# Kernel tuning notes

Hardware: AMD Instinct MI355X
Metric: run time of the kernel (lower is better)

Reference implementation:

```python
import jax, jax.numpy as jnp
import numpy as np

N = 50000      # nodes
E = 800000     # edges (avg degree 16)
C_IN = 64
C_OUT = 64
H = 32         # hidden_nf (hard-coded in module)
L = 4          # egnn_clean.EGNN default n_layers


def _lin(key, fan_in, fan_out):
    s = 1.0 / np.sqrt(fan_in)
    kw, kb = jax.random.split(key)
    w = jax.random.uniform(kw, (fan_in, fan_out), jnp.float32, -s, s)
    b = jax.random.uniform(kb, (fan_out,), jnp.float32, -s, s)
    return w, b


def _stack(key, fan_in, fan_out):
    ws, bs = zip(*[_lin(jax.random.fold_in(key, l), fan_in, fan_out) for l in range(L)])
    return jnp.stack(ws), jnp.stack(bs)


def setup_inputs() -> dict:
    key = jax.random.key(0)
    k = jax.random.split(key, 16)
    inp = {
        'data': jax.random.normal(k[0], (N, C_IN), jnp.float32),
        'pos': jax.random.normal(k[1], (N, 2), jnp.float32),
        'edge_attr': jax.random.normal(k[2], (E, 1), jnp.float32),
        't': jnp.ones((1,), jnp.float32),
        'row': jax.random.randint(k[3], (E,), 0, N),
        'col': jax.random.randint(k[4], (E,), 0, N),
    }
    inp['emb_in_w'], inp['emb_in_b'] = _lin(k[5], C_IN + 1, H)
    inp['emb_out_w'], inp['emb_out_b'] = _lin(k[6], H, C_OUT)
    inp['edge_w1'], inp['edge_b1'] = _stack(k[7], 2 * H + 2, H)  # [h_i, h_j, radial, edge_attr]
    inp['edge_w2'], inp['edge_b2'] = _stack(k[8], H, H)
    inp['node_w1'], inp['node_b1'] = _stack(k[9], 2 * H, H)
    inp['node_w2'], inp['node_b2'] = _stack(k[10], H, H)
    inp['coord_w1'], inp['coord_b1'] = _stack(k[11], H, H)
    lim = 0.001 * np.sqrt(6.0 / (H + 1))  # xavier_uniform gain=0.001, no bias
    inp['coord_w2'] = jax.random.uniform(k[12], (L, H, 1), jnp.float32, -lim, lim)
    return inp


def _egnn(data, pos, edge_attr, t, emb_in_w, emb_in_b, edge_w1, edge_b1, edge_w2, edge_b2,
          node_w1, node_b1, node_w2, node_b2, coord_w1, coord_b1, coord_w2,
          emb_out_w, emb_out_b, row, col):
    n = data.shape[0]
    silu = jax.nn.silu
    # prepend time channel; pad 2D coords with a zero z-column
    h = jnp.concatenate([jnp.broadcast_to(t.reshape(1, 1), (n, 1)), data], axis=1)  # [N, C_IN+1]
    x = jnp.concatenate([pos, jnp.zeros((n, 1), pos.dtype)], axis=1)                # [N, 3]
    h = h @ emb_in_w + emb_in_b                                                     # [N, H]
    ones_e = jnp.ones((row.shape[0], 1), x.dtype)
    cnt = jnp.maximum(jax.ops.segment_sum(ones_e, row, num_segments=n), 1.0)        # [N,1] clamp(min=1)
    for l in range(L):
        diff = x[row] - x[col]                                    # [E, 3]
        radial = jnp.sum(diff * diff, axis=1, keepdims=True)      # [E, 1]
        ein = jnp.concatenate([h[row], h[col], radial, edge_attr], axis=1)  # [E, 2H+2]
        m = silu(silu(ein @ edge_w1[l] + edge_b1[l]) @ edge_w2[l] + edge_b2[l])  # edge MLP [E, H]
        # equivariant coordinate update (coords_agg='mean')
        phi = silu(m @ coord_w1[l] + coord_b1[l]) @ coord_w2[l]   # [E, 1]
        x = x + jax.ops.segment_sum(diff * phi, row, num_segments=n) / cnt
        # node update (sum aggregation, residual)
        agg = jax.ops.segment_sum(m, row, num_segments=n)         # [N, H]
        upd = silu(jnp.concatenate([h, agg], axis=1) @ node_w1[l] + node_b1[l]) @ node_w2[l] + node_b2[l]
        h = h + upd
    return h @ emb_out_w + emb_out_b                              # [N, C_OUT]


def reference(data, pos, edge_attr, t, emb_in_w, emb_in_b, edge_w1, edge_b1, edge_w2, edge_b2,
              node_w1, node_b1, node_w2, node_b2, coord_w1, coord_b1, coord_w2,
              emb_out_w, emb_out_b, row, col):
    return _egnn(data, pos, edge_attr, t, emb_in_w, emb_in_b, edge_w1, edge_b1, edge_w2, edge_b2,
                 node_w1, node_b1, node_w2, node_b2, coord_w1, coord_b1, coord_w2,
                 emb_out_w, emb_out_b, row, col)
```

## Files before the change

### kernel.cpp

```cpp
#include <hip/hip_runtime.h>
#include <hip/hip_fp16.h>

#define NN 50000
#define NE 800000
#define CIN 64
#define COUT 64
#define HD 32
#define NL 4
#define NBUK 196
#define BUKSH 8
#define EPB 3125
#define MAXB 4864
#define BLKE 128

typedef float f32x4 __attribute__((ext_vector_type(4)));
typedef _Float16 half8 __attribute__((ext_vector_type(8)));

__device__ __forceinline__ float silu_f(float v) {
    return v * __builtin_amdgcn_rcpf(1.0f + __expf(-v));
}

__global__ __launch_bounds__(256) void embed_kernel(
    const float* __restrict__ data, const float* __restrict__ pos,
    const float* __restrict__ tptr,
    const float* __restrict__ W, const float* __restrict__ b,
    const float* __restrict__ eW1_0,
    float* __restrict__ h, float* __restrict__ x4,
    __half* __restrict__ Hrh, __half* __restrict__ Hch,
    int* __restrict__ bcnt, float* __restrict__ aggM, float* __restrict__ aggX4)
{
    int n = blockIdx.x * 256 + threadIdx.x;
    if (n >= NN) return;
    float t = tptr[0];
    float d[CIN];
    const float4* dp = (const float4*)(data + (size_t)n * CIN);
#pragma unroll
    for (int i = 0; i < CIN / 4; i++) {
        float4 v = dp[i];
        d[4*i+0] = v.x; d[4*i+1] = v.y; d[4*i+2] = v.z; d[4*i+3] = v.w;
    }
    float acc[HD];
#pragma unroll
    for (int j = 0; j < HD; j++) acc[j] = fmaf(t, W[j], b[j]);
#pragma unroll
    for (int i = 0; i < CIN; i++) {
        float a = d[i];
#pragma unroll
        for (int j = 0; j < HD; j++) acc[j] = fmaf(a, W[(i + 1) * HD + j], acc[j]);
    }
    float4* hp = (float4*)(h + (size_t)n * HD);
#pragma unroll
    for (int j = 0; j < HD / 4; j++)
        hp[j] = make_float4(acc[4*j], acc[4*j+1], acc[4*j+2], acc[4*j+3]);
    ((float4*)x4)[n] = make_float4(pos[n*2+0], pos[n*2+1], 0.0f, 0.0f);

    float a1[HD], a2[HD];
#pragma unroll
    for (int j = 0; j < HD; j++) { a1[j] = 0.0f; a2[j] = 0.0f; }
#pragma unroll
    for (int i = 0; i < HD; i++) {
        float z = acc[i];
#pragma unroll
        for (int j = 0; j < HD; j++) {
            a1[j] = fmaf(z, eW1_0[i * HD + j], a1[j]);
            a2[j] = fmaf(z, eW1_0[(HD + i) * HD + j], a2[j]);
        }
    }
    int w1[16], w2[16];
#pragma unroll
    for (int q = 0; q < 16; q++) {
        __half2 p1 = __floats2half2_rn(a1[2*q], a1[2*q+1]);
        __half2 p2 = __floats2half2_rn(a2[2*q], a2[2*q+1]);
        w1[q] = *(int*)&p1;
        w2[q] = *(int*)&p2;
    }
    int4* rp = (int4*)(Hrh + (size_t)n * HD);
    int4* cp = (int4*)(Hch + (size_t)n * HD);
#pragma unroll
    for (int q = 0; q < 4; q++) {
        rp[q] = make_int4(w1[4*q], w1[4*q+1], w1[4*q+2], w1[4*q+3]);
        cp[q] = make_int4(w2[4*q], w2[4*q+1], w2[4*q+2], w2[4*q+3]);
    }

    if (n < NBUK) bcnt[n] = 0;
    float4 z4 = make_float4(0.f, 0.f, 0.f, 0.f);
    float4* za = (float4*)(aggM + (size_t)n * HD);
#pragma unroll
    for (int j = 0; j < HD/4; j++) za[j] = z4;
    ((float4*)aggX4)[n] = z4;
}

__global__ __launch_bounds__(128) void prep_kernel(
    const float* __restrict__ eW2, const float* __restrict__ cW1,
    __half* __restrict__ w2B, __half* __restrict__ cW1B)
{
    int l  = blockIdx.x;
    int nt = threadIdx.x >> 6;
    int wl = threadIdx.x & 63;
    int rsel = wl & 15, ksel = wl >> 4;
#pragma unroll
    for (int e = 0; e < 8; e++) {
        int k = 8 * ksel + e;
        int j = 16 * nt + rsel;
        size_t o = ((size_t)(l * 2 + nt) * 64 + wl) * 8 + e;
        w2B[o]  = __float2half(eW2[(size_t)l * HD * HD + k * HD + j]);
        cW1B[o] = __float2half(cW1[(size_t)l * HD * HD + k * HD + j]);
    }
}

__global__ __launch_bounds__(256) void sortS1_kernel(
    const int* __restrict__ row, int* __restrict__ bcnt, int* __restrict__ resv)
{
    __shared__ int lb[256];
    int tid = threadIdx.x;
    lb[tid] = 0;
    __syncthreads();
    int base = blockIdx.x * EPB;
    for (int i = tid; i < EPB; i += 256)
        atomicAdd(&lb[row[base + i] >> BUKSH], 1);
    __syncthreads();
    if (tid < NBUK)
        resv[blockIdx.x * NBUK + tid] = atomicAdd(&bcnt[tid], lb[tid]);
}

__global__ __launch_bounds__(256) void sortS2_kernel(
    const int* __restrict__ bcnt, int* __restrict__ bbase)
{
    __shared__ int sd[256];
    int tid = threadIdx.x;
    int v = (tid < NBUK) ? bcnt[tid] : 0;
    sd[tid] = v;
    __syncthreads();
    for (int off = 1; off < 256; off <<= 1) {
        int t = (tid >= off) ? sd[tid - off] : 0;
        __syncthreads();
        sd[tid] += t;
        __syncthreads();
    }
    if (tid < NBUK) bbase[tid] = sd[tid] - v;
    if (tid == 255) bbase[NBUK] = sd[255];
}

__global__ __launch_bounds__(256) void sortS3_kernel(
    const int* __restrict__ row, const int* __restrict__ col,
    const float* __restrict__ eattr,
    const int* __restrict__ bbase, const int* __restrict__ resv,
    int4* __restrict__ tmp)
{
    __shared__ int4 st[EPB];
    __shared__ int lb[256];
    __shared__ int lbex[NBUK];
    __shared__ int lcur[NBUK];
    __shared__ int sd[256];
    int tid = threadIdx.x;
    int base = blockIdx.x * EPB;
    lb[tid] = 0;
    if (tid < NBUK) lcur[tid] = 0;
    __syncthreads();
    for (int i = tid; i < EPB; i += 256)
        atomicAdd(&lb[row[base + i] >> BUKSH], 1);
    __syncthreads();
    int v = lb[tid];
    sd[tid] = v;
    __syncthreads();
    for (int off = 1; off < 256; off <<= 1) {
        int t = (tid >= off) ? sd[tid - off] : 0;
        __syncthreads();
        sd[tid] += t;
        __syncthreads();
    }
    if (tid < NBUK) lbex[tid] = sd[tid] - v;
    __syncthreads();
    for (int i = tid; i < EPB; i += 256) {
        int e = base + i;
        int r = row[e];
        int b = r >> BUKSH;
        int p = lbex[b] + atomicAdd(&lcur[b], 1);
        st[p] = make_int4(r, col[e], __float_as_int(eattr[e]), 0);
    }
    __syncthreads();
    int wid = tid >> 6, lane = tid & 63;
    for (int k = wid; k < NBUK; k += 4) {
        int L = lb[k];
        int g = bbase[k] + resv[blockIdx.x * NBUK + k];
        int o = lbex[k];
        for (int i = lane; i < L; i += 64)
            tmp[g + i] = st[o + i];
    }
}

__global__ __launch_bounds__(256) void sortS4_kernel(
    const int4* __restrict__ tmp, const int* __restrict__ bbase,
    int4* __restrict__ sedge, int* __restrict__ rowstart)
{
    __shared__ int4 st[MAXB];
    __shared__ int lcnt[256], lex[256], lcur[256], sd[256];
    int tid = threadIdx.x;
    int k = blockIdx.x;
    int lo = bbase[k], hi = bbase[k + 1];
    int nE = hi - lo;
    int nodeBase = k << BUKSH;
    lcnt[tid] = 0; lcur[tid] = 0;
    __syncthreads();
    for (int i = tid; i < nE; i += 256)
        atomicAdd(&lcnt[tmp[lo + i].x - nodeBase], 1);
    __syncthreads();
    int v = lcnt[tid];
    sd[tid] = v;
    __syncthreads();
    for (int off = 1; off < 256; off <<= 1) {
        int t = (tid >= off) ? sd[tid - off] : 0;
        __syncthreads();
        sd[tid] += t;
        __syncthreads();
    }
    lex[tid] = sd[tid] - v;
    int n = nodeBase + tid;
    if (n < NN) rowstart[n] = lo + lex[tid];
    if (k == NBUK - 1 && tid == 0) rowstart[NN] = NE;
    __syncthreads();
    for (int i = tid; i < nE; i += 256) {
        int4 e = tmp[lo + i];
        int ln = e.x - nodeBase;
        int p = lex[ln] + atomicAdd(&lcur[ln], 1);
        st[p] = e;
    }
    __syncthreads();
    for (int i = tid; i < nE; i += 256)
        sedge[lo + i] = st[i];
}

__global__ __launch_bounds__(128, 8) void edge_fused_kernel(
    const float* __restrict__ x4,
    const int4* __restrict__ sedge,
    const __half* __restrict__ Hrh, const __half* __restrict__ Hch,
    const float* __restrict__ eW1, const float* __restrict__ eb1,
    const float* __restrict__ eb2,
    const __half* __restrict__ w2Bl, const __half* __restrict__ cW1Bl,
    const float* __restrict__ cb1, const float* __restrict__ cW2,
    const int* __restrict__ rowstart,
    float* __restrict__ aggM, float* __restrict__ aggX4)
{
    __shared__ __align__(16) __half At[BLKE][40];
    __shared__ __half sx[BLKE][4];
    __shared__ float  phib[BLKE];
    __shared__ int snf, snl;
    int tid = threadIdx.x;
    int s_base = blockIdx.x * BLKE;
    int s = s_base + tid;
    int4 ei = sedge[s];
    int r = ei.x, c = ei.y;
    float ea = __int_as_float(ei.z);
    if (tid == 0)        snf = r;
    if (tid == BLKE - 1) snl = r;

    float4 xr = ((const float4*)x4)[r];
    float4 xc = ((const float4*)x4)[c];
    float d0 = xr.x - xc.x, d1 = xr.y - xc.y, d2 = xr.z - xc.z;
    float radial = d0*d0 + d1*d1 + d2*d2;

    const half8* hr8 = (const half8*)(Hrh + (size_t)r * HD);
    const half8* hc8 = (const half8*)(Hch + (size_t)c * HD);
    int wbuf[16];
#pragma unroll
    for (int i = 0; i < 4; i++) {
        half8 s8 = hr8[i] + hc8[i];
#pragma unroll
        for (int kk = 0; kk < 8; kk += 2) {
            int j = 8*i + kk;
            float v0 = (float)s8[kk]   + eb1[j]   + radial * eW1[64*HD+j]   + ea * eW1[65*HD+j];
            float v1 = (float)s8[kk+1] + eb1[j+1] + radial * eW1[64*HD+j+1] + ea * eW1[65*HD+j+1];
            __half2 p = __floats2half2_rn(silu_f(v0), silu_f(v1));
            wbuf[(j >> 1)] = *(int*)&p;
        }
    }
    int4* arow = (int4*)&At[tid][0];
#pragma unroll
    for (int q = 0; q < 4; q++)
        arow[q] = make_int4(wbuf[4*q], wbuf[4*q+1], wbuf[4*q+2], wbuf[4*q+3]);

    int wl = tid & 63;
    int wbase = tid & 64;
    int rsel = wl & 15, ksel = wl >> 4;

    half8 bw0 = ((const half8*)w2Bl)[wl];
    half8 bw1 = ((const half8*)w2Bl)[64 + wl];
    float bc0 = eb2[rsel], bc1 = eb2[16 + rsel];
    f32x4 acc[4][2];
#pragma unroll
    for (int mt = 0; mt < 4; mt++) {
        acc[mt][0] = (f32x4){bc0, bc0, bc0, bc0};
        acc[mt][1] = (f32x4){bc1, bc1, bc1, bc1};
    }
#pragma unroll
    for (int mt = 0; mt < 4; mt++) {
        half8 af = *(const half8*)&At[wbase + 16*mt + rsel][8*ksel];
        acc[mt][0] = __builtin_amdgcn_mfma_f32_16x16x32_f16(af, bw0, acc[mt][0], 0, 0, 0);
        acc[mt][1] = __builtin_amdgcn_mfma_f32_16x16x32_f16(af, bw1, acc[mt][1], 0, 0, 0);
    }
#pragma unroll
    for (int mt = 0; mt < 4; mt++)
#pragma unroll
        for (int nt = 0; nt < 2; nt++)
#pragma unroll
            for (int q = 0; q < 4; q++) {
                float mv = silu_f(acc[mt][nt][q]);
                At[wbase + 16*mt + 4*ksel + q][16*nt + rsel] = __float2half(mv);
            }

    half8 cw0 = ((const half8*)cW1Bl)[wl];
    half8 cw1 = ((const half8*)cW1Bl)[64 + wl];
    float cc0 = cb1[rsel], cc1 = cb1[16 + rsel];
    f32x4 cacc[4][2];
#pragma unroll
    for (int mt = 0; mt < 4; mt++) {
        cacc[mt][0] = (f32x4){cc0, cc0, cc0, cc0};
        cacc[mt][1] = (f32x4){cc1, cc1, cc1, cc1};
    }
#pragma unroll
    for (int mt = 0; mt < 4; mt++) {
        half8 am = *(const half8*)&At[wbase + 16*mt + rsel][8*ksel];
        cacc[mt][0] = __builtin_amdgcn_mfma_f32_16x16x32_f16(am, cw0, cacc[mt][0], 0, 0, 0);
        cacc[mt][1] = __builtin_amdgcn_mfma_f32_16x16x32_f16(am, cw1, cacc[mt][1], 0, 0, 0);
    }

    float cw2a = cW2[rsel], cw2b = cW2[16 + rsel];
    float p[4][4];
#pragma unroll
    for (int mt = 0; mt < 4; mt++)
#pragma unroll
        for (int q = 0; q < 4; q++)
            p[mt][q] = silu_f(cacc[mt][0][q]) * cw2a + silu_f(cacc[mt][1][q]) * cw2b;
#pragma unroll
    for (int dd = 1; dd < 16; dd <<= 1)
#pragma unroll
        for (int mt = 0; mt < 4; mt++)
#pragma unroll
            for (int q = 0; q < 4; q++)
                p[mt][q] += __shfl_xor(p[mt][q], dd);
    if (rsel == 0) {
#pragma unroll
        for (int mt = 0; mt < 4; mt++)
#pragma unroll
            for (int q = 0; q < 4; q++)
                phib[wbase + 16*mt + 4*ksel + q] = p[mt][q];
    }
    float phi = phib[tid];

    *(__half2*)&sx[tid][0] = __floats2half2_rn(d0 * phi, d1 * phi);
    sx[tid][2] = __float2half(d2 * phi);
    __syncthreads();

    int g = tid >> 5, ch = tid & 31;
    int nf = snf, nl = snl;
    for (int node = nf + g; node <= nl; node += 4) {
        int lo = rowstart[node], hi = rowstart[node + 1];
        int clo = lo - s_base; if (clo < 0) clo = 0;
        int chi = hi - s_base; if (chi > BLKE) chi = BLKE;
        if (chi <= clo) continue;
        float am = 0.0f;
        for (int j = clo; j < chi; j++) am += __half2float(At[j][ch]);
        bool interior = (lo >= s_base) && (hi <= s_base + BLKE);
        if (interior) aggM[(size_t)node * HD + ch] = am;
        else          atomicAdd(&aggM[(size_t)node * HD + ch], am);
        if (ch < 3) {
            float ax = 0.0f;
            for (int j = clo; j < chi; j++) ax += __half2float(sx[j][ch]);
            if (interior) aggX4[(size_t)node * 4 + ch] = ax;
            else          atomicAdd(&aggX4[(size_t)node * 4 + ch], ax);
        }
    }
}

__global__ __launch_bounds__(256) void node_fused_kernel(
    float* __restrict__ h, float* __restrict__ x4,
    float* __restrict__ aggM, float* __restrict__ aggX4,
    const int* __restrict__ rowstart,
    const float* __restrict__ nW1, const float* __restrict__ nb1,
    const float* __restrict__ nW2, const float* __restrict__ nb2,
    const float* __restrict__ eW1n,
    __half* __restrict__ Hrh, __half* __restrict__ Hch,
    const float* __restrict__ Wout, const float* __restrict__ bout,
    float* __restrict__ out)
{
    __shared__ float sIn[8][2*HD];
    __shared__ float sU[8][HD];
    __shared__ float sH[8][HD];
    int local = threadIdx.x >> 5;
    int ch    = threadIdx.x & 31;
    int n = blockIdx.x * 8 + local;
    float hv = h[(size_t)n * HD + ch];
    float am = aggM[(size_t)n * HD + ch];
    aggM[(size_t)n * HD + ch] = 0.0f;
    sIn[local][ch]      = hv;
    sIn[local][HD + ch] = am;
    if (ch < 3) {
        int cnt = rowstart[n + 1] - rowstart[n];
        float cf = (cnt < 1) ? 1.0f : (float)cnt;
        x4[(size_t)n * 4 + ch] += aggX4[(size_t)n * 4 + ch] / cf;
        aggX4[(size_t)n * 4 + ch] = 0.0f;
    }
    __syncthreads();
    float u1 = nb1[ch];
#pragma unroll 8
    for (int i = 0; i < 2*HD; i++) u1 = fmaf(sIn[local][i], nW1[i * HD + ch], u1);
    u1 = silu_f(u1);
    sU[local][ch] = u1;
    __syncthreads();
    float u2 = nb2[ch];
#pragma unroll 8
    for (int i = 0; i < HD; i++) u2 = fmaf(sU[local][i], nW2[i * HD + ch], u2);
    float hn = hv + u2;

    if (eW1n != nullptr) {
        h[(size_t)n * HD + ch] = hn;
        sH[local][ch] = hn;
        __syncthreads();
        float a = 0.0f, b = 0.0f;
#pragma unroll 8
        for (int i = 0; i < HD; i++) {
            float z = sH[local][i];
            a = fmaf(z, eW1n[i * HD + ch], a);
            b = fmaf(z, eW1n[(HD + i) * HD + ch], b);
        }
        Hrh[(size_t)n * HD + ch] = __float2half(a);
        Hch[(size_t)n * HD + ch] = __float2half(b);
    } else {
        sH[local][ch] = hn;
        __syncthreads();
        float o0 = bout[ch], o1 = bout[HD + ch];
#pragma unroll 8
        for (int i = 0; i < HD; i++) {
            float z = sH[local][i];
            o0 = fmaf(z, Wout[i * COUT + ch], o0);
            o1 = fmaf(z, Wout[i * COUT + HD + ch], o1);
        }
        out[(size_t)n * COUT + ch]      = o0;
        out[(size_t)n * COUT + HD + ch] = o1;
    }
}

extern "C" void kernel_launch(void* const* d_in, const int* in_sizes, int n_in,
                              void* d_out, int out_size, void* d_ws, size_t ws_size,
                              hipStream_t stream) {
    const float* data      = (const float*)d_in[0];
    const float* pos       = (const float*)d_in[1];
    const float* edge_attr = (const float*)d_in[2];
    const float* tptr      = (const float*)d_in[3];
    const int*   row       = (const int*)d_in[4];
    const int*   col       = (const int*)d_in[5];
    const float* emb_in_w  = (const float*)d_in[6];
    const float* emb_in_b  = (const float*)d_in[7];
    const float* emb_out_w = (const float*)d_in[8];
    const float* emb_out_b = (const float*)d_in[9];
    const float* edge_w1   = (const float*)d_in[10];
    const float* edge_b1   = (const float*)d_in[11];
    const float* edge_w2   = (const float*)d_in[12];
    const float* edge_b2   = (const float*)d_in[13];
    const float* node_w1   = (const float*)d_in[14];
    const float* node_b1   = (const float*)d_in[15];
    const float* node_w2   = (const float*)d_in[16];
    const float* node_b2   = (const float*)d_in[17];
    const float* coord_w1  = (const float*)d_in[18];
    const float* coord_b1  = (const float*)d_in[19];
    const float* coord_w2  = (const float*)d_in[20];
    float* out = (float*)d_out;

    float* ws = (float*)d_ws;
    float* h      = ws;
    float* x4     = ws + 1600000;
    __half* Hrh   = (__half*)(ws + 1800000);
    __half* Hch   = (__half*)(ws + 2600000);
    float* aggM   = ws + 3400000;
    float* aggX4  = ws + 5000000;
    int* rowstart = (int*)(ws + 5200000);
    int* bcnt     = (int*)(ws + 5250004);
    int* bbase    = (int*)(ws + 5250204);
    int* resv     = (int*)(ws + 5250404);
    int4* sedge   = (int4*)(ws + 5400000);
    int4* tmp     = (int4*)(ws + 8600000);
    __half* w2B   = (__half*)(ws + 11800000);
    __half* cW1B  = w2B + (size_t)NL * 1024;

    embed_kernel<<<(NN + 255) / 256, 256, 0, stream>>>(
        data, pos, tptr, emb_in_w, emb_in_b, edge_w1 ,
        h, x4, Hrh, Hch, bcnt, aggM, aggX4);
    prep_kernel<<<NL, 128, 0, stream>>>(edge_w2, coord_w1, w2B, cW1B);
    sortS1_kernel<<<256, 256, 0, stream>>>(row, bcnt, resv);
    sortS2_kernel<<<1, 256, 0, stream>>>(bcnt, bbase);
    sortS3_kernel<<<256, 256, 0, stream>>>(row, col, edge_attr, bbase, resv, tmp);
    sortS4_kernel<<<NBUK, 256, 0, stream>>>(tmp, bbase, sedge, rowstart);

    for (int l = 0; l < NL; l++) {
        edge_fused_kernel<<<NE / BLKE, BLKE, 0, stream>>>(
            x4, sedge, Hrh, Hch,
            edge_w1 + l * (2*HD+2) * HD, edge_b1 + l * HD,
            edge_b2 + l * HD,
            w2B + (size_t)l * 1024, cW1B + (size_t)l * 1024,
            coord_b1 + l * HD, coord_w2 + l * HD,
            rowstart, aggM, aggX4);
        bool lastl = (l + 1 == NL);
        node_fused_kernel<<<NN / 8, 256, 0, stream>>>(
            h, x4, aggM, aggX4, rowstart,
            node_w1 + l * 2 * HD * HD, node_b1 + l * HD,
            node_w2 + l * HD * HD,     node_b2 + l * HD,
            lastl ? nullptr : (edge_w1 + (l + 1) * (2*HD+2) * HD), Hrh, Hch,
            emb_out_w, emb_out_b, lastl ? out : nullptr);
    }
}
```

Measured before the change: 413.3 us.

## Merge prologue kernels and compute bucket offsets inside scatter kernel

Combines embedding, per-block bucket histogram and weight repacking into one prologue launch, and removes the global atomic counter and separate scan kernel. Each scatter block now recomputes global bucket totals and its own prefix by reading all per-block histograms, which cuts three launches and their serialization. The cost is redundant reads of the histogram table in every block, and the histogram pass over rows is no longer repeated in the scatter kernel. It also raises wave priority around the MFMA sections in the edge kernel.

```diff
diff --git a/kernel.cpp b/kernel.cpp
--- a/kernel.cpp
+++ b/kernel.cpp
@@ -12,6 +12,7 @@
 #define EPB 3125
 #define MAXB 4864
 #define BLKE 128
+#define EMB_BLKS 196
 
 typedef float f32x4 __attribute__((ext_vector_type(4)));
 typedef _Float16 half8 __attribute__((ext_vector_type(8)));
@@ -20,148 +21,127 @@
     return v * __builtin_amdgcn_rcpf(1.0f + __expf(-v));
 }
 
-__global__ __launch_bounds__(256) void embed_kernel(
+__global__ __launch_bounds__(256) void prologue_kernel(
     const float* __restrict__ data, const float* __restrict__ pos,
     const float* __restrict__ tptr,
     const float* __restrict__ W, const float* __restrict__ b,
     const float* __restrict__ eW1_0,
+    const int* __restrict__ row,
+    const float* __restrict__ eW2, const float* __restrict__ cW1,
     float* __restrict__ h, float* __restrict__ x4,
     __half* __restrict__ Hrh, __half* __restrict__ Hch,
-    int* __restrict__ bcnt, float* __restrict__ aggM, float* __restrict__ aggX4)
-{
-    int n = blockIdx.x * 256 + threadIdx.x;
-    if (n >= NN) return;
-    float t = tptr[0];
-    float d[CIN];
-    const float4* dp = (const float4*)(data + (size_t)n * CIN);
-#pragma unroll
-    for (int i = 0; i < CIN / 4; i++) {
-        float4 v = dp[i];
-        d[4*i+0] = v.x; d[4*i+1] = v.y; d[4*i+2] = v.z; d[4*i+3] = v.w;
-    }
-    float acc[HD];
-#pragma unroll
-    for (int j = 0; j < HD; j++) acc[j] = fmaf(t, W[j], b[j]);
-#pragma unroll
-    for (int i = 0; i < CIN; i++) {
-        float a = d[i];
-#pragma unroll
-        for (int j = 0; j < HD; j++) acc[j] = fmaf(a, W[(i + 1) * HD + j], acc[j]);
-    }
-    float4* hp = (float4*)(h + (size_t)n * HD);
-#pragma unroll
-    for (int j = 0; j < HD / 4; j++)
-        hp[j] = make_float4(acc[4*j], acc[4*j+1], acc[4*j+2], acc[4*j+3]);
-    ((float4*)x4)[n] = make_float4(pos[n*2+0], pos[n*2+1], 0.0f, 0.0f);
-
-    float a1[HD], a2[HD];
-#pragma unroll
-    for (int j = 0; j < HD; j++) { a1[j] = 0.0f; a2[j] = 0.0f; }
-#pragma unroll
-    for (int i = 0; i < HD; i++) {
-        float z = acc[i];
-#pragma unroll
-        for (int j = 0; j < HD; j++) {
-            a1[j] = fmaf(z, eW1_0[i * HD + j], a1[j]);
-            a2[j] = fmaf(z, eW1_0[(HD + i) * HD + j], a2[j]);
-        }
-    }
-    int w1[16], w2[16];
-#pragma unroll
-    for (int q = 0; q < 16; q++) {
-        __half2 p1 = __floats2half2_rn(a1[2*q], a1[2*q+1]);
-        __half2 p2 = __floats2half2_rn(a2[2*q], a2[2*q+1]);
-        w1[q] = *(int*)&p1;
-        w2[q] = *(int*)&p2;
-    }
-    int4* rp = (int4*)(Hrh + (size_t)n * HD);
-    int4* cp = (int4*)(Hch + (size_t)n * HD);
-#pragma unroll
-    for (int q = 0; q < 4; q++) {
-        rp[q] = make_int4(w1[4*q], w1[4*q+1], w1[4*q+2], w1[4*q+3]);
-        cp[q] = make_int4(w2[4*q], w2[4*q+1], w2[4*q+2], w2[4*q+3]);
-    }
-
-    if (n < NBUK) bcnt[n] = 0;
-    float4 z4 = make_float4(0.f, 0.f, 0.f, 0.f);
-    float4* za = (float4*)(aggM + (size_t)n * HD);
-#pragma unroll
-    for (int j = 0; j < HD/4; j++) za[j] = z4;
-    ((float4*)aggX4)[n] = z4;
-}
-
-__global__ __launch_bounds__(128) void prep_kernel(
-    const float* __restrict__ eW2, const float* __restrict__ cW1,
+    float* __restrict__ aggM, float* __restrict__ aggX4,
+    int* __restrict__ resv,
     __half* __restrict__ w2B, __half* __restrict__ cW1B)
 {
-    int l  = blockIdx.x;
-    int nt = threadIdx.x >> 6;
-    int wl = threadIdx.x & 63;
-    int rsel = wl & 15, ksel = wl >> 4;
-#pragma unroll
-    for (int e = 0; e < 8; e++) {
-        int k = 8 * ksel + e;
-        int j = 16 * nt + rsel;
-        size_t o = ((size_t)(l * 2 + nt) * 64 + wl) * 8 + e;
-        w2B[o]  = __float2half(eW2[(size_t)l * HD * HD + k * HD + j]);
-        cW1B[o] = __float2half(cW1[(size_t)l * HD * HD + k * HD + j]);
-    }
-}
-
-__global__ __launch_bounds__(256) void sortS1_kernel(
-    const int* __restrict__ row, int* __restrict__ bcnt, int* __restrict__ resv)
-{
-    __shared__ int lb[256];
+    int blk = blockIdx.x;
     int tid = threadIdx.x;
-    lb[tid] = 0;
-    __syncthreads();
-    int base = blockIdx.x * EPB;
-    for (int i = tid; i < EPB; i += 256)
-        atomicAdd(&lb[row[base + i] >> BUKSH], 1);
-    __syncthreads();
-    if (tid < NBUK)
-        resv[blockIdx.x * NBUK + tid] = atomicAdd(&bcnt[tid], lb[tid]);
-}
-
-__global__ __launch_bounds__(256) void sortS2_kernel(
-    const int* __restrict__ bcnt, int* __restrict__ bbase)
-{
-    __shared__ int sd[256];
-    int tid = threadIdx.x;
-    int v = (tid < NBUK) ? bcnt[tid] : 0;
-    sd[tid] = v;
-    __syncthreads();
-    for (int off = 1; off < 256; off <<= 1) {
-        int t = (tid >= off) ? sd[tid - off] : 0;
-        __syncthreads();
-        sd[tid] += t;
-        __syncthreads();
-    }
-    if (tid < NBUK) bbase[tid] = sd[tid] - v;
-    if (tid == 255) bbase[NBUK] = sd[255];
+
+    if (blk < EMB_BLKS) {
+        int n = blk * 256 + tid;
+        if (n >= NN) return;
+        float t = tptr[0];
+        float d[CIN];
+        const float4* dp = (const float4*)(data + (size_t)n * CIN);
+#pragma unroll
+        for (int i = 0; i < CIN / 4; i++) {
+            float4 v = dp[i];
+            d[4*i+0] = v.x; d[4*i+1] = v.y; d[4*i+2] = v.z; d[4*i+3] = v.w;
+        }
+        float acc[HD];
+#pragma unroll
+        for (int j = 0; j < HD; j++) acc[j] = fmaf(t, W[j], b[j]);
+#pragma unroll
+        for (int i = 0; i < CIN; i++) {
+            float a = d[i];
+#pragma unroll
+            for (int j = 0; j < HD; j++) acc[j] = fmaf(a, W[(i + 1) * HD + j], acc[j]);
+        }
+        float4* hp = (float4*)(h + (size_t)n * HD);
+#pragma unroll
+        for (int j = 0; j < HD / 4; j++)
+            hp[j] = make_float4(acc[4*j], acc[4*j+1], acc[4*j+2], acc[4*j+3]);
+        ((float4*)x4)[n] = make_float4(pos[n*2+0], pos[n*2+1], 0.0f, 0.0f);
+
+        float a1[HD], a2[HD];
+#pragma unroll
+        for (int j = 0; j < HD; j++) { a1[j] = 0.0f; a2[j] = 0.0f; }
+#pragma unroll
+        for (int i = 0; i < HD; i++) {
+            float z = acc[i];
+#pragma unroll
+            for (int j = 0; j < HD; j++) {
+                a1[j] = fmaf(z, eW1_0[i * HD + j], a1[j]);
+                a2[j] = fmaf(z, eW1_0[(HD + i) * HD + j], a2[j]);
+            }
+        }
+        int w1[16], w2[16];
+#pragma unroll
+        for (int q = 0; q < 16; q++) {
+            __half2 p1 = __floats2half2_rn(a1[2*q], a1[2*q+1]);
+            __half2 p2 = __floats2half2_rn(a2[2*q], a2[2*q+1]);
+            w1[q] = *(int*)&p1;
+            w2[q] = *(int*)&p2;
+        }
+        int4* rp = (int4*)(Hrh + (size_t)n * HD);
+        int4* cp = (int4*)(Hch + (size_t)n * HD);
+#pragma unroll
+        for (int q = 0; q < 4; q++) {
+            rp[q] = make_int4(w1[4*q], w1[4*q+1], w1[4*q+2], w1[4*q+3]);
+            cp[q] = make_int4(w2[4*q], w2[4*q+1], w2[4*q+2], w2[4*q+3]);
+        }
+        float4 z4 = make_float4(0.f, 0.f, 0.f, 0.f);
+        float4* za = (float4*)(aggM + (size_t)n * HD);
+#pragma unroll
+        for (int j = 0; j < HD/4; j++) za[j] = z4;
+        ((float4*)aggX4)[n] = z4;
+    } else if (blk < EMB_BLKS + 256) {
+        __shared__ int lb[256];
+        int sb = blk - EMB_BLKS;
+        lb[tid] = 0;
+        __syncthreads();
+        int base = sb * EPB;
+        for (int i = tid; i < EPB; i += 256)
+            atomicAdd(&lb[row[base + i] >> BUKSH], 1);
+        __syncthreads();
+        if (tid < NBUK) resv[sb * NBUK + tid] = lb[tid];
+    } else {
+        if (tid >= 128) return;
+        int nt = tid >> 6;
+        int wl = tid & 63;
+        int rsel = wl & 15, ksel = wl >> 4;
+        for (int l = 0; l < NL; l++) {
+#pragma unroll
+            for (int e = 0; e < 8; e++) {
+                int k = 8 * ksel + e;
+                int j = 16 * nt + rsel;
+                size_t o = ((size_t)(l * 2 + nt) * 64 + wl) * 8 + e;
+                w2B[o]  = __float2half(eW2[(size_t)l * HD * HD + k * HD + j]);
+                cW1B[o] = __float2half(cW1[(size_t)l * HD * HD + k * HD + j]);
+            }
+        }
+    }
 }
 
 __global__ __launch_bounds__(256) void sortS3_kernel(
     const int* __restrict__ row, const int* __restrict__ col,
     const float* __restrict__ eattr,
-    const int* __restrict__ bbase, const int* __restrict__ resv,
-    int4* __restrict__ tmp)
+    const int* __restrict__ resv,
+    int4* __restrict__ tmp, int* __restrict__ bbase_g)
 {
     __shared__ int4 st[EPB];
-    __shared__ int lb[256];
-    __shared__ int lbex[NBUK];
+    __shared__ int sd[256];
+    __shared__ int lcnt_s[NBUK];
+    __shared__ int lbex_s[NBUK];
+    __shared__ int g_s[NBUK];
     __shared__ int lcur[NBUK];
-    __shared__ int sd[256];
     int tid = threadIdx.x;
-    int base = blockIdx.x * EPB;
-    lb[tid] = 0;
-    if (tid < NBUK) lcur[tid] = 0;
-    __syncthreads();
-    for (int i = tid; i < EPB; i += 256)
-        atomicAdd(&lb[row[base + i] >> BUKSH], 1);
-    __syncthreads();
-    int v = lb[tid];
-    sd[tid] = v;
+    int bb = blockIdx.x;
+    int base = bb * EPB;
+
+    int myCnt = (tid < NBUK) ? resv[bb * NBUK + tid] : 0;
+    if (tid < NBUK) { lcnt_s[tid] = myCnt; lcur[tid] = 0; }
+    sd[tid] = myCnt;
     __syncthreads();
     for (int off = 1; off < 256; off <<= 1) {
         int t = (tid >= off) ? sd[tid - off] : 0;
@@ -169,21 +149,46 @@
         sd[tid] += t;
         __syncthreads();
     }
-    if (tid < NBUK) lbex[tid] = sd[tid] - v;
-    __syncthreads();
+    if (tid < NBUK) lbex_s[tid] = sd[tid] - myCnt;
+    __syncthreads();
+
+    int tot = 0, pre = 0;
+    if (tid < NBUK) {
+        for (int b2 = 0; b2 < 256; b2++) {
+            int cv = resv[b2 * NBUK + tid];
+            tot += cv;
+            if (b2 < bb) pre += cv;
+        }
+    }
+    sd[tid] = (tid < NBUK) ? tot : 0;
+    __syncthreads();
+    for (int off = 1; off < 256; off <<= 1) {
+        int t = (tid >= off) ? sd[tid - off] : 0;
+        __syncthreads();
+        sd[tid] += t;
+        __syncthreads();
+    }
+    if (tid < NBUK) {
+        int bbase_k = sd[tid] - tot;
+        g_s[tid] = bbase_k + pre;
+        if (bb == 0) bbase_g[tid] = bbase_k;
+    }
+    if (bb == 0 && tid == 255) bbase_g[NBUK] = sd[255];
+    __syncthreads();
+
     for (int i = tid; i < EPB; i += 256) {
         int e = base + i;
         int r = row[e];
-        int b = r >> BUKSH;
-        int p = lbex[b] + atomicAdd(&lcur[b], 1);
+        int bk = r >> BUKSH;
+        int p = lbex_s[bk] + atomicAdd(&lcur[bk], 1);
         st[p] = make_int4(r, col[e], __float_as_int(eattr[e]), 0);
     }
     __syncthreads();
     int wid = tid >> 6, lane = tid & 63;
     for (int k = wid; k < NBUK; k += 4) {
-        int L = lb[k];
-        int g = bbase[k] + resv[blockIdx.x * NBUK + k];
-        int o = lbex[k];
+        int L = lcnt_s[k];
+        int g = g_s[k];
+        int o = lbex_s[k];
         for (int i = lane; i < L; i += 64)
             tmp[g + i] = st[o + i];
     }
@@ -292,12 +297,14 @@
         acc[mt][0] = (f32x4){bc0, bc0, bc0, bc0};
         acc[mt][1] = (f32x4){bc1, bc1, bc1, bc1};
     }
+    __builtin_amdgcn_s_setprio(1);
 #pragma unroll
     for (int mt = 0; mt < 4; mt++) {
         half8 af = *(const half8*)&At[wbase + 16*mt + rsel][8*ksel];
         acc[mt][0] = __builtin_amdgcn_mfma_f32_16x16x32_f16(af, bw0, acc[mt][0], 0, 0, 0);
         acc[mt][1] = __builtin_amdgcn_mfma_f32_16x16x32_f16(af, bw1, acc[mt][1], 0, 0, 0);
     }
+    __builtin_amdgcn_s_setprio(0);
 #pragma unroll
     for (int mt = 0; mt < 4; mt++)
 #pragma unroll
@@ -317,12 +324,14 @@
         cacc[mt][0] = (f32x4){cc0, cc0, cc0, cc0};
         cacc[mt][1] = (f32x4){cc1, cc1, cc1, cc1};
     }
+    __builtin_amdgcn_s_setprio(1);
 #pragma unroll
     for (int mt = 0; mt < 4; mt++) {
         half8 am = *(const half8*)&At[wbase + 16*mt + rsel][8*ksel];
         cacc[mt][0] = __builtin_amdgcn_mfma_f32_16x16x32_f16(am, cw0, cacc[mt][0], 0, 0, 0);
         cacc[mt][1] = __builtin_amdgcn_mfma_f32_16x16x32_f16(am, cw1, cacc[mt][1], 0, 0, 0);
     }
+    __builtin_amdgcn_s_setprio(0);
 
     float cw2a = cW2[rsel], cw2b = cW2[16 + rsel];
     float p[4][4];
@@ -474,7 +483,6 @@
     float* aggM   = ws + 3400000;
     float* aggX4  = ws + 5000000;
     int* rowstart = (int*)(ws + 5200000);
-    int* bcnt     = (int*)(ws + 5250004);
     int* bbase    = (int*)(ws + 5250204);
     int* resv     = (int*)(ws + 5250404);
     int4* sedge   = (int4*)(ws + 5400000);
@@ -482,13 +490,11 @@
     __half* w2B   = (__half*)(ws + 11800000);
     __half* cW1B  = w2B + (size_t)NL * 1024;
 
-    embed_kernel<<<(NN + 255) / 256, 256, 0, stream>>>(
+    prologue_kernel<<<EMB_BLKS + 256 + 1, 256, 0, stream>>>(
         data, pos, tptr, emb_in_w, emb_in_b, edge_w1 ,
-        h, x4, Hrh, Hch, bcnt, aggM, aggX4);
-    prep_kernel<<<NL, 128, 0, stream>>>(edge_w2, coord_w1, w2B, cW1B);
-    sortS1_kernel<<<256, 256, 0, stream>>>(row, bcnt, resv);
-    sortS2_kernel<<<1, 256, 0, stream>>>(bcnt, bbase);
-    sortS3_kernel<<<256, 256, 0, stream>>>(row, col, edge_attr, bbase, resv, tmp);
+        row, edge_w2, coord_w1,
+        h, x4, Hrh, Hch, aggM, aggX4, resv, w2B, cW1B);
+    sortS3_kernel<<<256, 256, 0, stream>>>(row, col, edge_attr, resv, tmp, bbase);
     sortS4_kernel<<<NBUK, 256, 0, stream>>>(tmp, bbase, sedge, rowstart);
 
     for (int l = 0; l < NL; l++) {
```

Measured after the change: 410.6 us (median of 2 runs). About the same (-0.6%).
